# Kernel tuning notes

Measured on AMD Instinct MI355X. Metric: run time of the kernel, lower is better.

The kernel has to match this reference:

```python
import jax, jax.numpy as jnp
import numpy as np

D_MODEL = 1024
H = 16
D_K = D_MODEL // H
B = 2
S = 2048


def setup_inputs() -> dict:
    key = jax.random.key(0)
    ks = jax.random.split(key, 11)
    scale = 1.0 / np.sqrt(D_MODEL)
    inp = {
        "query": jax.random.normal(ks[0], (B, S, D_MODEL), jnp.float32),
        "key_in": jax.random.normal(ks[1], (B, S, D_MODEL), jnp.float32),
        "value": jax.random.normal(ks[2], (B, S, D_MODEL), jnp.float32),
        # causal mask, broadcast over heads: 1 = keep, 0 = masked
        "mask": jnp.tril(jnp.ones((S, S), jnp.int32))[None, None, :, :].repeat(B, axis=0),
        "w_q": jax.random.normal(ks[3], (D_MODEL, D_MODEL), jnp.float32) * scale,
        "b_q": jax.random.normal(ks[4], (D_MODEL,), jnp.float32) * 0.01,
        "w_k": jax.random.normal(ks[5], (D_MODEL, D_MODEL), jnp.float32) * scale,
        "b_k": jax.random.normal(ks[6], (D_MODEL,), jnp.float32) * 0.01,
        "w_v": jax.random.normal(ks[7], (D_MODEL, D_MODEL), jnp.float32) * scale,
        "b_v": jax.random.normal(ks[8], (D_MODEL,), jnp.float32) * 0.01,
        "w_out": jax.random.normal(ks[9], (D_MODEL, D_MODEL), jnp.float32) * scale,
        "b_out": jax.random.normal(ks[10], (D_MODEL,), jnp.float32) * 0.01,
    }
    return inp


def _split_heads(x):
    # [B,S,D] -> [B,H,S,d_k]
    b, s, _ = x.shape
    return x.reshape(b, s, H, D_K).transpose(0, 2, 1, 3)


def reference(query, key_in, value, mask, w_q, b_q, w_k, b_k, w_v, b_v, w_out, b_out):
    q = _split_heads(query @ w_q.T + b_q)
    k = _split_heads(key_in @ w_k.T + b_k)
    v = _split_heads(value @ w_v.T + b_v)
    scores = jnp.einsum("bhqd,bhkd->bhqk", q, k) / jnp.sqrt(jnp.float32(D_K))
    scores = jnp.where(mask == 0, jnp.float32(-1e9), scores)
    attn = jax.nn.softmax(scores, axis=-1)  # dropout rate 0.0 -> identity
    out = jnp.einsum("bhqk,bhkd->bhqd", attn, v)
    out = out.transpose(0, 2, 1, 3).reshape(query.shape[0], -1, D_MODEL)
    return out @ w_out.T + b_out
```

## Files before the change

kernel.cpp:

```cpp
#include <hip/hip_runtime.h>
#include <hip/hip_bf16.h>

#define D_MODEL 1024
#define NH 16
#define DKH 64
#define BB 2
#define SS 2048
#define MTOT (BB * SS)

typedef __hip_bfloat16 bf16;
typedef __attribute__((ext_vector_type(8))) short short8;
typedef __attribute__((ext_vector_type(4))) short short4v;
typedef __attribute__((ext_vector_type(4))) float floatx4;

__device__ __forceinline__ bf16 f2bf(float x) { return __float2bfloat16(x); }

__device__ __forceinline__ void async_cp16(const void* g, void* l) {
  __builtin_amdgcn_global_load_lds(
      (const __attribute__((address_space(1))) unsigned int*)g,
      (__attribute__((address_space(3))) unsigned int*)l, 16, 0, 0);
}

__global__ __launch_bounds__(256) void convert_kernel(
    const float* __restrict__ wq, const float* __restrict__ wk,
    const float* __restrict__ wv, const float* __restrict__ wo,
    const float* __restrict__ qi, const float* __restrict__ ki,
    const float* __restrict__ vi, bf16* __restrict__ Wb,
    bf16* __restrict__ Qi, bf16* __restrict__ Ki, bf16* __restrict__ Vi) {
  const int id = blockIdx.x * 256 + threadIdx.x;
  const float* src;
  bf16* dst;
  if (id < (1 << 20)) {
    const int m = id >> 18, loc = id & 0x3FFFF;
    src = ((m == 0) ? wq : (m == 1) ? wk : (m == 2) ? wv : wo) + (size_t)loc * 4;
    dst = Wb + ((size_t)m << 20) + (size_t)loc * 4;
  } else {
    const int t = id - (1 << 20);
    const int m = t >> 20, loc = t & 0xFFFFF;
    src = ((m == 0) ? qi : (m == 1) ? ki : vi) + (size_t)loc * 4;
    dst = ((m == 0) ? Qi : (m == 1) ? Ki : Vi) + (size_t)loc * 4;
  }
  const float4 v = *(const float4*)src;
  short4v s;
  bf16* pb = (bf16*)&s;
  pb[0] = f2bf(v.x); pb[1] = f2bf(v.y); pb[2] = f2bf(v.z); pb[3] = f2bf(v.w);
  *(short4v*)dst = s;
}

__device__ __forceinline__ void gemm_qkv_body(const bf16* __restrict__ A,
                                              const bf16* __restrict__ W,
                                              const float* __restrict__ Bi,
                                              bf16* __restrict__ C, int mode) {
  constexpr int N = 1024, K = 1024;
  __shared__ bf16 As[2][128 * 32];
  __shared__ bf16 Ws[2][128 * 32];

  const int tid = threadIdx.x;
  const int w = tid >> 6, lane = tid & 63, quad = lane >> 4, n16 = lane & 15;
  const int bx = blockIdx.x;
  const int bm = bx & 31, bn = bx >> 5;
  const int wm = (w & 1) * 64, wn = (w >> 1) * 64;

  const int rb = lane >> 2, cb = lane & 3;
  const int gsw = (cb ^ ((rb >> 1) & 3)) * 8;
  const int rkey = ((n16 >> 1) & 3) * 8;

  const bf16* Ag0 = A + (size_t)(bm * 128) * K;
  const bf16* Wg0 = W + (size_t)(bn * 128) * K;

  auto issue = [&](int buf, int k0) {
#pragma unroll
    for (int ii = 0; ii < 2; ii++) {
      const int R = w * 32 + ii * 16 + rb;
      async_cp16(Ag0 + (size_t)R * K + k0 + gsw,
                 (void*)&As[buf][(w * 32 + ii * 16) * 32]);
      async_cp16(Wg0 + (size_t)R * K + k0 + gsw,
                 (void*)&Ws[buf][(w * 32 + ii * 16) * 32]);
    }
  };

  floatx4 acc[4][4] = {};
  issue(0, 0);
  int buf = 0;
  for (int k0 = 0; k0 < K; k0 += 32) {
    __syncthreads();
    if (k0 + 32 < K) issue(buf ^ 1, k0 + 32);

    short8 af[4], bfr[4];
#pragma unroll
    for (int i = 0; i < 4; i++)
      af[i] = *(const short8*)(&As[buf][(wm + i * 16 + n16) * 32 + ((quad * 8) ^ rkey)]);
#pragma unroll
    for (int j = 0; j < 4; j++)
      bfr[j] = *(const short8*)(&Ws[buf][(wn + j * 16 + n16) * 32 + ((quad * 8) ^ rkey)]);
#pragma unroll
    for (int i = 0; i < 4; i++)
#pragma unroll
      for (int j = 0; j < 4; j++)
        acc[i][j] = __builtin_amdgcn_mfma_f32_16x16x32_bf16(af[i], bfr[j], acc[i][j], 0, 0, 0);
    buf ^= 1;
  }

  float bv[4];
#pragma unroll
  for (int j = 0; j < 4; j++) bv[j] = Bi[bn * 128 + wn + j * 16 + n16];

#pragma unroll
  for (int i = 0; i < 4; i++) {
    const int rowb = bm * 128 + wm + i * 16 + quad * 4;
#pragma unroll
    for (int j = 0; j < 4; j++) {
      const int col = bn * 128 + wn + j * 16 + n16;
      if (mode == 1) {
        short4v s;
        bf16* pb = (bf16*)&s;
#pragma unroll
        for (int r = 0; r < 4; r++) pb[r] = f2bf(acc[i][j][r] + bv[j]);
        *(short4v*)(C + (size_t)col * MTOT + rowb) = s;
      } else {
#pragma unroll
        for (int r = 0; r < 4; r++)
          C[(size_t)(rowb + r) * N + col] = f2bf(acc[i][j][r] + bv[j]);
      }
    }
  }
}

__global__ __launch_bounds__(256) void gemm_qkv_kernel(
    const bf16* __restrict__ Qi, const bf16* __restrict__ Ki,
    const bf16* __restrict__ Vi, const bf16* __restrict__ Wb,
    const float* __restrict__ bq, const float* __restrict__ bk,
    const float* __restrict__ bv, bf16* __restrict__ Qw,
    bf16* __restrict__ Kw, bf16* __restrict__ VTw) {
  const int z = blockIdx.z;
  const bf16* A = (z == 0) ? Qi : (z == 1) ? Ki : Vi;
  const bf16* W = Wb + ((size_t)z << 20);
  const float* Bi = (z == 0) ? bq : (z == 1) ? bk : bv;
  bf16* C = (z == 0) ? Qw : (z == 1) ? Kw : VTw;
  gemm_qkv_body(A, W, Bi, C, (z == 2) ? 1 : 0);
}

__global__ __launch_bounds__(256) void gemm_out_kernel(
    const bf16* __restrict__ A, const bf16* __restrict__ W,
    const float* __restrict__ Bi, float* __restrict__ C) {
  constexpr int N = 1024, K = 1024;
  __shared__ bf16 As[2][64 * 32];
  __shared__ bf16 Ws[2][64 * 32];

  const int tid = threadIdx.x;
  const int w = tid >> 6, lane = tid & 63, quad = lane >> 4, n16 = lane & 15;
  const int bx = blockIdx.x;
  const int bm = bx & 63, bn = bx >> 6;
  const int wm = w * 16;

  const int rb = lane >> 2, cb = lane & 3;
  const int gsw = (cb ^ ((rb >> 1) & 3)) * 8;
  const int rkey = ((n16 >> 1) & 3) * 8;

  const bf16* Ag0 = A + (size_t)(bm * 64) * K;
  const bf16* Wg0 = W + (size_t)(bn * 64) * K;

  auto issue = [&](int buf, int kk) {
    const int R = w * 16 + rb;
    async_cp16(Ag0 + (size_t)R * K + kk + gsw, (void*)&As[buf][(w * 16) * 32]);
    async_cp16(Wg0 + (size_t)R * K + kk + gsw, (void*)&Ws[buf][(w * 16) * 32]);
  };

  floatx4 acc[4] = {};
  issue(0, 0);
  int buf = 0;
  for (int k0 = 0; k0 < K; k0 += 32) {
    __syncthreads();
    if (k0 + 32 < K) issue(buf ^ 1, k0 + 32);

    short8 af = *(const short8*)(&As[buf][(wm + n16) * 32 + ((quad * 8) ^ rkey)]);
#pragma unroll
    for (int j = 0; j < 4; j++) {
      short8 bfr = *(const short8*)(&Ws[buf][(j * 16 + n16) * 32 + ((quad * 8) ^ rkey)]);
      acc[j] = __builtin_amdgcn_mfma_f32_16x16x32_bf16(af, bfr, acc[j], 0, 0, 0);
    }
    buf ^= 1;
  }

  float bv[4];
#pragma unroll
  for (int j = 0; j < 4; j++) bv[j] = Bi[bn * 64 + j * 16 + n16];

  const int rowb = bm * 64 + wm + quad * 4;
#pragma unroll
  for (int j = 0; j < 4; j++) {
    const int col = bn * 64 + j * 16 + n16;
#pragma unroll
    for (int r = 0; r < 4; r++)
      C[(size_t)(rowb + r) * N + col] = acc[j][r] + bv[j];
  }
}

__global__ __launch_bounds__(256, 2) void attn_kernel(const bf16* __restrict__ Q,
                                                      const bf16* __restrict__ Kg,
                                                      const bf16* __restrict__ VT,
                                                      bf16* __restrict__ O) {
  constexpr int BN = 128;
  __shared__ bf16 Ks[2][128 * 64];
  __shared__ bf16 Vs[2][64 * 128];
  __shared__ bf16 Pw[4][16 * 128];

  const int tid = threadIdx.x;
  const int w = tid >> 6, lane = tid & 63, quad = lane >> 4, n16 = lane & 15;
  const int hb = blockIdx.x;
  const int h = hb & 15, b = hb >> 4, p = blockIdx.y;
  const size_t qoff = (size_t)b * SS * D_MODEL + h * DKH;
  const bf16* VTh = VT + (size_t)(h * DKH) * MTOT + (size_t)b * SS;

  const int kvr = tid >> 3, ck = tid & 7;
  const int dd = tid >> 4, cv = tid & 15;
  const int wk = (kvr & 7) << 3;
  const int wv = (dd & 7) << 3;
  const int swz = (n16 & 7) << 3;

  short8 kreg[4], vreg[4];
  auto loadKV = [&](int kv0) {
#pragma unroll
    for (int ii = 0; ii < 4; ii++) {
      kreg[ii] = *(const short8*)(Kg + qoff + (size_t)(kv0 + ii * 32 + kvr) * D_MODEL + ck * 8);
      vreg[ii] = *(const short8*)(VTh + (size_t)(ii * 16 + dd) * MTOT + kv0 + cv * 8);
    }
  };

  bf16* pwb = &Pw[w][0];
  loadKV(0);
  int buf = 0;

  for (int hf = 0; hf < 2; hf++) {
    const int q0 = (hf == 0) ? p * 64 : (31 - p) * 64;
    const int q0w = q0 + w * 16;
    const int nt = (q0 + 191) >> 7;

    short8 aQ0, aQ1;
    {
      const bf16* qp = Q + qoff + (size_t)(q0w + n16) * D_MODEL + quad * 8;
      aQ0 = *(const short8*)(qp);
      aQ1 = *(const short8*)(qp + 32);
    }

    floatx4 facc[4] = {};
    float lsum = 0.f;

    for (int t = 0; t < nt; t++) {
#pragma unroll
      for (int ii = 0; ii < 4; ii++) {
        *(short8*)(&Ks[buf][(ii * 32 + kvr) * 64 + ((ck * 8) ^ wk)]) = kreg[ii];
        *(short8*)(&Vs[buf][(ii * 16 + dd) * 128 + ((cv * 8) ^ wv)]) = vreg[ii];
      }
      if (t + 1 < nt) loadKV((t + 1) * BN);
      else if (hf == 0) loadKV(0);
      __syncthreads();

      const int kv0 = t * BN;
      const bool lastT = (t == nt - 1);
      const bf16* ksb = &Ks[buf][0];

#pragma unroll
      for (int blk = 0; blk < 8; blk++) {
        const int krow = blk * 16 + n16;
        short8 ak0 = *(const short8*)(ksb + krow * 64 + ((quad * 8) ^ swz));
        short8 ak1 = *(const short8*)(ksb + krow * 64 + ((quad * 8 + 32) ^ swz));
        floatx4 z = {};
        z = __builtin_amdgcn_mfma_f32_16x16x32_bf16(ak0, aQ0, z, 0, 0, 0);
        z = __builtin_amdgcn_mfma_f32_16x16x32_bf16(ak1, aQ1, z, 0, 0, 0);
        short4v s;
        bf16* pb = (bf16*)&s;
        if (lastT) {
          const int kbase = kv0 + blk * 16 + quad * 4, qcol = q0w + n16;
#pragma unroll
          for (int r = 0; r < 4; r++) {
            float pe = __expf(z[r] * 0.125f);
            if (kbase + r > qcol) pe = 0.f;
            lsum += pe;
            pb[r] = f2bf(pe);
          }
        } else {
#pragma unroll
          for (int r = 0; r < 4; r++) {
            const float pe = __expf(z[r] * 0.125f);
            lsum += pe;
            pb[r] = f2bf(pe);
          }
        }
        *(short4v*)(pwb + n16 * 128 + ((blk * 16 + quad * 4) ^ swz)) = s;
      }

      short8 aP[4];
#pragma unroll
      for (int c = 0; c < 4; c++)
        aP[c] = *(const short8*)(pwb + n16 * 128 + ((c * 32 + quad * 8) ^ swz));

      const bf16* vsb = &Vs[buf][0];
      __builtin_amdgcn_s_setprio(1);
#pragma unroll
      for (int d = 0; d < 4; d++)
#pragma unroll
        for (int c = 0; c < 4; c++) {
          short8 bvf = *(const short8*)(vsb + (d * 16 + n16) * 128 + ((c * 32 + quad * 8) ^ swz));
          facc[d] = __builtin_amdgcn_mfma_f32_16x16x32_bf16(aP[c], bvf, facc[d], 0, 0, 0);
        }
      __builtin_amdgcn_s_setprio(0);
      buf ^= 1;
    }

    lsum += __shfl_xor(lsum, 16);
    lsum += __shfl_xor(lsum, 32);
#pragma unroll
    for (int r = 0; r < 4; r++) {
      const float linv = 1.f / __shfl(lsum, quad * 4 + r);
      const int qrow = q0w + quad * 4 + r;
      bf16* op = O + qoff + (size_t)qrow * D_MODEL;
#pragma unroll
      for (int d = 0; d < 4; d++) op[d * 16 + n16] = f2bf(facc[d][r] * linv);
    }
  }
}

extern "C" void kernel_launch(void* const* d_in, const int* in_sizes, int n_in,
                              void* d_out, int out_size, void* d_ws, size_t ws_size,
                              hipStream_t stream) {
  (void)in_sizes; (void)n_in; (void)out_size; (void)ws_size;
  const float* query  = (const float*)d_in[0];
  const float* key_in = (const float*)d_in[1];
  const float* value  = (const float*)d_in[2];
  const float* w_q = (const float*)d_in[4];
  const float* b_q = (const float*)d_in[5];
  const float* w_k = (const float*)d_in[6];
  const float* b_k = (const float*)d_in[7];
  const float* w_v = (const float*)d_in[8];
  const float* b_v = (const float*)d_in[9];
  const float* w_o = (const float*)d_in[10];
  const float* b_o = (const float*)d_in[11];
  float* outp = (float*)d_out;

  const size_t mat = (size_t)MTOT * D_MODEL;
  bf16* Qws  = (bf16*)d_ws;
  bf16* Kws  = Qws + mat;
  bf16* VTws = Kws + mat;
  bf16* Wb   = VTws + mat;
  bf16* Vi   = Wb + 4 * (size_t)(1 << 20);
  bf16* Qi = (bf16*)d_out;
  bf16* Ki = Qi + mat;

  convert_kernel<<<16384, 256, 0, stream>>>(w_q, w_k, w_v, w_o, query, key_in,
                                            value, Wb, Qi, Ki, Vi);

  dim3 gq(256, 1, 3);
  gemm_qkv_kernel<<<gq, 256, 0, stream>>>(Qi, Ki, Vi, Wb, b_q, b_k, b_v, Qws,
                                          Kws, VTws);
  dim3 ga(NH * BB, 16);
  attn_kernel<<<ga, 256, 0, stream>>>(Qws, Kws, VTws, Qws);
  gemm_out_kernel<<<1024, 256, 0, stream>>>(Qws, Wb + ((size_t)3 << 20), b_o, outp);
}
```

Before: 232.4 us.

## Shrink attention KV tile, drop paired q-blocks, enlarge output GEMM M-tile

The attention kernel now handles one 64-row query block per workgroup instead of pairing a light and a heavy block. It uses 64-wide KV tiles with smaller LDS buffers and asks for 4 workgroups per CU through launch bounds, which doubles the attention grid and gives finer causal tiles with less masked waste. The output projection GEMM moves to 128x64 tiles with two A fragments per wave, so each B fragment loaded from LDS is reused twice and the grid is halved. The risks are load imbalance across the causal q-blocks, since the heaviest-first ordering now relies on the scheduler, and register pressure under the higher occupancy bound.

```diff
diff --git a/kernel.cpp b/kernel.cpp
--- a/kernel.cpp
+++ b/kernel.cpp
@@ -144,180 +144,188 @@
     const bf16* __restrict__ A, const bf16* __restrict__ W,
     const float* __restrict__ Bi, float* __restrict__ C) {
   constexpr int N = 1024, K = 1024;
-  __shared__ bf16 As[2][64 * 32];
+  __shared__ bf16 As[2][128 * 32];
   __shared__ bf16 Ws[2][64 * 32];
 
   const int tid = threadIdx.x;
   const int w = tid >> 6, lane = tid & 63, quad = lane >> 4, n16 = lane & 15;
   const int bx = blockIdx.x;
-  const int bm = bx & 63, bn = bx >> 6;
-  const int wm = w * 16;
+  const int bm = bx & 31, bn = bx >> 5;
+  const int wm = w * 32;
 
   const int rb = lane >> 2, cb = lane & 3;
   const int gsw = (cb ^ ((rb >> 1) & 3)) * 8;
   const int rkey = ((n16 >> 1) & 3) * 8;
 
-  const bf16* Ag0 = A + (size_t)(bm * 64) * K;
+  const bf16* Ag0 = A + (size_t)(bm * 128) * K;
   const bf16* Wg0 = W + (size_t)(bn * 64) * K;
 
   auto issue = [&](int buf, int kk) {
-    const int R = w * 16 + rb;
-    async_cp16(Ag0 + (size_t)R * K + kk + gsw, (void*)&As[buf][(w * 16) * 32]);
-    async_cp16(Wg0 + (size_t)R * K + kk + gsw, (void*)&Ws[buf][(w * 16) * 32]);
+#pragma unroll
+    for (int ii = 0; ii < 2; ii++) {
+      const int R = w * 32 + ii * 16 + rb;
+      async_cp16(Ag0 + (size_t)R * K + kk + gsw,
+                 (void*)&As[buf][(w * 32 + ii * 16) * 32]);
+    }
+    const int Rw = w * 16 + rb;
+    async_cp16(Wg0 + (size_t)Rw * K + kk + gsw, (void*)&Ws[buf][(w * 16) * 32]);
   };
 
-  floatx4 acc[4] = {};
+  floatx4 acc[2][4] = {};
   issue(0, 0);
   int buf = 0;
   for (int k0 = 0; k0 < K; k0 += 32) {
     __syncthreads();
     if (k0 + 32 < K) issue(buf ^ 1, k0 + 32);
 
-    short8 af = *(const short8*)(&As[buf][(wm + n16) * 32 + ((quad * 8) ^ rkey)]);
+    short8 af[2], bfr[4];
+#pragma unroll
+    for (int i = 0; i < 2; i++)
+      af[i] = *(const short8*)(&As[buf][(wm + i * 16 + n16) * 32 + ((quad * 8) ^ rkey)]);
+#pragma unroll
+    for (int j = 0; j < 4; j++)
+      bfr[j] = *(const short8*)(&Ws[buf][(j * 16 + n16) * 32 + ((quad * 8) ^ rkey)]);
+#pragma unroll
+    for (int i = 0; i < 2; i++)
+#pragma unroll
+      for (int j = 0; j < 4; j++)
+        acc[i][j] = __builtin_amdgcn_mfma_f32_16x16x32_bf16(af[i], bfr[j], acc[i][j], 0, 0, 0);
+    buf ^= 1;
+  }
+
+  float bv[4];
+#pragma unroll
+  for (int j = 0; j < 4; j++) bv[j] = Bi[bn * 64 + j * 16 + n16];
+
+#pragma unroll
+  for (int i = 0; i < 2; i++) {
+    const int rowb = bm * 128 + wm + i * 16 + quad * 4;
 #pragma unroll
     for (int j = 0; j < 4; j++) {
-      short8 bfr = *(const short8*)(&Ws[buf][(j * 16 + n16) * 32 + ((quad * 8) ^ rkey)]);
-      acc[j] = __builtin_amdgcn_mfma_f32_16x16x32_bf16(af, bfr, acc[j], 0, 0, 0);
-    }
-    buf ^= 1;
-  }
-
-  float bv[4];
-#pragma unroll
-  for (int j = 0; j < 4; j++) bv[j] = Bi[bn * 64 + j * 16 + n16];
-
-  const int rowb = bm * 64 + wm + quad * 4;
-#pragma unroll
-  for (int j = 0; j < 4; j++) {
-    const int col = bn * 64 + j * 16 + n16;
-#pragma unroll
-    for (int r = 0; r < 4; r++)
-      C[(size_t)(rowb + r) * N + col] = acc[j][r] + bv[j];
-  }
-}
-
-__global__ __launch_bounds__(256, 2) void attn_kernel(const bf16* __restrict__ Q,
+      const int col = bn * 64 + j * 16 + n16;
+#pragma unroll
+      for (int r = 0; r < 4; r++)
+        C[(size_t)(rowb + r) * N + col] = acc[i][j][r] + bv[j];
+    }
+  }
+}
+
+__global__ __launch_bounds__(256, 4) void attn_kernel(const bf16* __restrict__ Q,
                                                       const bf16* __restrict__ Kg,
                                                       const bf16* __restrict__ VT,
                                                       bf16* __restrict__ O) {
-  constexpr int BN = 128;
-  __shared__ bf16 Ks[2][128 * 64];
-  __shared__ bf16 Vs[2][64 * 128];
-  __shared__ bf16 Pw[4][16 * 128];
+  constexpr int BN = 64;
+  __shared__ bf16 Ks[2][64 * 64];
+  __shared__ bf16 Vs[2][64 * 64];
+  __shared__ bf16 Pw[4][16 * 64];
 
   const int tid = threadIdx.x;
   const int w = tid >> 6, lane = tid & 63, quad = lane >> 4, n16 = lane & 15;
   const int hb = blockIdx.x;
-  const int h = hb & 15, b = hb >> 4, p = blockIdx.y;
+  const int h = hb & 15, b = hb >> 4;
+  const int q0 = (31 - (int)blockIdx.y) * 64;
   const size_t qoff = (size_t)b * SS * D_MODEL + h * DKH;
   const bf16* VTh = VT + (size_t)(h * DKH) * MTOT + (size_t)b * SS;
 
   const int kvr = tid >> 3, ck = tid & 7;
-  const int dd = tid >> 4, cv = tid & 15;
-  const int wk = (kvr & 7) << 3;
-  const int wv = (dd & 7) << 3;
+  const int wkey = (kvr & 7) << 3;
   const int swz = (n16 & 7) << 3;
 
-  short8 kreg[4], vreg[4];
+  short8 kreg[2], vreg[2];
   auto loadKV = [&](int kv0) {
 #pragma unroll
-    for (int ii = 0; ii < 4; ii++) {
+    for (int ii = 0; ii < 2; ii++) {
       kreg[ii] = *(const short8*)(Kg + qoff + (size_t)(kv0 + ii * 32 + kvr) * D_MODEL + ck * 8);
-      vreg[ii] = *(const short8*)(VTh + (size_t)(ii * 16 + dd) * MTOT + kv0 + cv * 8);
+      vreg[ii] = *(const short8*)(VTh + (size_t)(ii * 32 + kvr) * MTOT + kv0 + ck * 8);
     }
   };
 
   bf16* pwb = &Pw[w][0];
+  const int q0w = q0 + w * 16;
+  const int nt = q0 / 64 + 1;
+
+  short8 aQ0, aQ1;
+  {
+    const bf16* qp = Q + qoff + (size_t)(q0w + n16) * D_MODEL + quad * 8;
+    aQ0 = *(const short8*)(qp);
+    aQ1 = *(const short8*)(qp + 32);
+  }
+
+  floatx4 facc[4] = {};
+  float lsum = 0.f;
+
   loadKV(0);
   int buf = 0;
-
-  for (int hf = 0; hf < 2; hf++) {
-    const int q0 = (hf == 0) ? p * 64 : (31 - p) * 64;
-    const int q0w = q0 + w * 16;
-    const int nt = (q0 + 191) >> 7;
-
-    short8 aQ0, aQ1;
-    {
-      const bf16* qp = Q + qoff + (size_t)(q0w + n16) * D_MODEL + quad * 8;
-      aQ0 = *(const short8*)(qp);
-      aQ1 = *(const short8*)(qp + 32);
-    }
-
-    floatx4 facc[4] = {};
-    float lsum = 0.f;
-
-    for (int t = 0; t < nt; t++) {
-#pragma unroll
-      for (int ii = 0; ii < 4; ii++) {
-        *(short8*)(&Ks[buf][(ii * 32 + kvr) * 64 + ((ck * 8) ^ wk)]) = kreg[ii];
-        *(short8*)(&Vs[buf][(ii * 16 + dd) * 128 + ((cv * 8) ^ wv)]) = vreg[ii];
+  for (int t = 0; t < nt; t++) {
+#pragma unroll
+    for (int ii = 0; ii < 2; ii++) {
+      *(short8*)(&Ks[buf][(ii * 32 + kvr) * 64 + ((ck * 8) ^ wkey)]) = kreg[ii];
+      *(short8*)(&Vs[buf][(ii * 32 + kvr) * 64 + ((ck * 8) ^ wkey)]) = vreg[ii];
+    }
+    if (t + 1 < nt) loadKV((t + 1) * BN);
+    __syncthreads();
+
+    const int kv0 = t * BN;
+    const bool lastT = (t == nt - 1);
+    const bf16* ksb = &Ks[buf][0];
+
+#pragma unroll
+    for (int blk = 0; blk < 4; blk++) {
+      const int krow = blk * 16 + n16;
+      short8 ak0 = *(const short8*)(ksb + krow * 64 + ((quad * 8) ^ swz));
+      short8 ak1 = *(const short8*)(ksb + krow * 64 + ((quad * 8 + 32) ^ swz));
+      floatx4 z = {};
+      z = __builtin_amdgcn_mfma_f32_16x16x32_bf16(ak0, aQ0, z, 0, 0, 0);
+      z = __builtin_amdgcn_mfma_f32_16x16x32_bf16(ak1, aQ1, z, 0, 0, 0);
+      short4v s;
+      bf16* pb = (bf16*)&s;
+      if (lastT) {
+        const int kbase = kv0 + blk * 16 + quad * 4, qcol = q0w + n16;
+#pragma unroll
+        for (int r = 0; r < 4; r++) {
+          float pe = __expf(z[r] * 0.125f);
+          if (kbase + r > qcol) pe = 0.f;
+          lsum += pe;
+          pb[r] = f2bf(pe);
+        }
+      } else {
+#pragma unroll
+        for (int r = 0; r < 4; r++) {
+          const float pe = __expf(z[r] * 0.125f);
+          lsum += pe;
+          pb[r] = f2bf(pe);
+        }
       }
-      if (t + 1 < nt) loadKV((t + 1) * BN);
-      else if (hf == 0) loadKV(0);
-      __syncthreads();
-
-      const int kv0 = t * BN;
-      const bool lastT = (t == nt - 1);
-      const bf16* ksb = &Ks[buf][0];
-
-#pragma unroll
-      for (int blk = 0; blk < 8; blk++) {
-        const int krow = blk * 16 + n16;
-        short8 ak0 = *(const short8*)(ksb + krow * 64 + ((quad * 8) ^ swz));
-        short8 ak1 = *(const short8*)(ksb + krow * 64 + ((quad * 8 + 32) ^ swz));
-        floatx4 z = {};
-        z = __builtin_amdgcn_mfma_f32_16x16x32_bf16(ak0, aQ0, z, 0, 0, 0);
-        z = __builtin_amdgcn_mfma_f32_16x16x32_bf16(ak1, aQ1, z, 0, 0, 0);
-        short4v s;
-        bf16* pb = (bf16*)&s;
-        if (lastT) {
-          const int kbase = kv0 + blk * 16 + quad * 4, qcol = q0w + n16;
-#pragma unroll
-          for (int r = 0; r < 4; r++) {
-            float pe = __expf(z[r] * 0.125f);
-            if (kbase + r > qcol) pe = 0.f;
-            lsum += pe;
-            pb[r] = f2bf(pe);
-          }
-        } else {
-#pragma unroll
-          for (int r = 0; r < 4; r++) {
-            const float pe = __expf(z[r] * 0.125f);
-            lsum += pe;
-            pb[r] = f2bf(pe);
-          }
-        }
-        *(short4v*)(pwb + n16 * 128 + ((blk * 16 + quad * 4) ^ swz)) = s;
+      *(short4v*)(pwb + n16 * 64 + ((blk * 16 + quad * 4) ^ swz)) = s;
+    }
+
+    short8 aP[2];
+#pragma unroll
+    for (int c = 0; c < 2; c++)
+      aP[c] = *(const short8*)(pwb + n16 * 64 + ((c * 32 + quad * 8) ^ swz));
+
+    const bf16* vsb = &Vs[buf][0];
+    __builtin_amdgcn_s_setprio(1);
+#pragma unroll
+    for (int d = 0; d < 4; d++)
+#pragma unroll
+      for (int c = 0; c < 2; c++) {
+        short8 bvf = *(const short8*)(vsb + (d * 16 + n16) * 64 + ((c * 32 + quad * 8) ^ swz));
+        facc[d] = __builtin_amdgcn_mfma_f32_16x16x32_bf16(aP[c], bvf, facc[d], 0, 0, 0);
       }
-
-      short8 aP[4];
-#pragma unroll
-      for (int c = 0; c < 4; c++)
-        aP[c] = *(const short8*)(pwb + n16 * 128 + ((c * 32 + quad * 8) ^ swz));
-
-      const bf16* vsb = &Vs[buf][0];
-      __builtin_amdgcn_s_setprio(1);
-#pragma unroll
-      for (int d = 0; d < 4; d++)
-#pragma unroll
-        for (int c = 0; c < 4; c++) {
-          short8 bvf = *(const short8*)(vsb + (d * 16 + n16) * 128 + ((c * 32 + quad * 8) ^ swz));
-          facc[d] = __builtin_amdgcn_mfma_f32_16x16x32_bf16(aP[c], bvf, facc[d], 0, 0, 0);
-        }
-      __builtin_amdgcn_s_setprio(0);
-      buf ^= 1;
-    }
-
-    lsum += __shfl_xor(lsum, 16);
-    lsum += __shfl_xor(lsum, 32);
-#pragma unroll
-    for (int r = 0; r < 4; r++) {
-      const float linv = 1.f / __shfl(lsum, quad * 4 + r);
-      const int qrow = q0w + quad * 4 + r;
-      bf16* op = O + qoff + (size_t)qrow * D_MODEL;
-#pragma unroll
-      for (int d = 0; d < 4; d++) op[d * 16 + n16] = f2bf(facc[d][r] * linv);
-    }
+    __builtin_amdgcn_s_setprio(0);
+    buf ^= 1;
+  }
+
+  lsum += __shfl_xor(lsum, 16);
+  lsum += __shfl_xor(lsum, 32);
+#pragma unroll
+  for (int r = 0; r < 4; r++) {
+    const float linv = 1.f / __shfl(lsum, quad * 4 + r);
+    const int qrow = q0w + quad * 4 + r;
+    bf16* op = O + qoff + (size_t)qrow * D_MODEL;
+#pragma unroll
+    for (int d = 0; d < 4; d++) op[d * 16 + n16] = f2bf(facc[d][r] * linv);
   }
 }
 
@@ -353,7 +361,7 @@
   dim3 gq(256, 1, 3);
   gemm_qkv_kernel<<<gq, 256, 0, stream>>>(Qi, Ki, Vi, Wb, b_q, b_k, b_v, Qws,
                                           Kws, VTws);
-  dim3 ga(NH * BB, 16);
+  dim3 ga(NH * BB, 32);
   attn_kernel<<<ga, 256, 0, stream>>>(Qws, Kws, VTws, Qws);
-  gemm_out_kernel<<<1024, 256, 0, stream>>>(Qws, Wb + ((size_t)3 << 20), b_o, outp);
-}
+  gemm_out_kernel<<<512, 256, 0, stream>>>(Qws, Wb + ((size_t)3 << 20), b_o, outp);
+}
```

After: 230.4 us. Within noise of the previous version (-0.9%).
